# Performance work log

Measured on AMD Instinct MI355X. Metric: run time of the kernel, lower is better.

Reference implementation:

```python
import jax, jax.numpy as jnp
import numpy as np

N = 100000
E = 1000000
IN_C = 256
HID = 64
OUT = 64
NEG_SLOPE = 0.2


def setup_inputs() -> dict:
    key = jax.random.key(0)
    ks = jax.random.split(key, 12)
    x = jax.random.normal(ks[0], (N, IN_C), dtype=jnp.float32)
    edge_index = jax.random.randint(ks[1], (2, E), 0, N, dtype=jnp.int64)
    s = 1.0 / np.sqrt(IN_C)
    W1 = jax.random.uniform(ks[2], (IN_C, HID), jnp.float32, -s, s)
    a1_src = jax.random.uniform(ks[3], (HID,), jnp.float32, -s, s)
    a1_dst = jax.random.uniform(ks[4], (HID,), jnp.float32, -s, s)
    b1 = jnp.zeros((HID,), jnp.float32)
    s2 = 1.0 / np.sqrt(HID)
    W2 = jax.random.uniform(ks[5], (HID, OUT), jnp.float32, -s2, s2)
    a2_src = jax.random.uniform(ks[6], (OUT,), jnp.float32, -s2, s2)
    a2_dst = jax.random.uniform(ks[7], (OUT,), jnp.float32, -s2, s2)
    b2 = jnp.zeros((OUT,), jnp.float32)
    return {"x": x, "edge_index": edge_index, "W1": W1, "a1_src": a1_src,
            "a1_dst": a1_dst, "b1": b1, "W2": W2, "a2_src": a2_src,
            "a2_dst": a2_dst, "b2": b2}


def gat_conv(x, W, a_src, a_dst, b, src, dst):
    h = x @ W                              # [N, d]
    alpha_s = h @ a_src                    # [N]
    alpha_d = h @ a_dst                    # [N]
    e = jax.nn.leaky_relu(alpha_s[src] + alpha_d[dst], NEG_SLOPE)  # [E]
    # segment softmax over incoming edges of each destination node
    e_max = jax.lax.stop_gradient(jax.ops.segment_max(e, dst, num_segments=N))
    ex = jnp.exp(e - e_max[dst])
    denom = jax.ops.segment_sum(ex, dst, num_segments=N)
    alpha = ex / (denom[dst] + 1e-16)      # [E]
    out = jax.ops.segment_sum(alpha[:, None] * h[src], dst, num_segments=N)
    return out + b


def reference(x, edge_index, W1, a1_src, a1_dst, b1, W2, a2_src, a2_dst, b2):
    src, dst = edge_index[0], edge_index[1]
    # dropout(p=0.6) is identity in eval mode
    h = jax.nn.relu(gat_conv(x, W1, a1_src, a1_dst, b1, src, dst))
    out = gat_conv(h, W2, a2_src, a2_dst, b2, src, dst)
    return out
```

## Files before the change

kernel.cpp:

```cpp
#include <hip/hip_runtime.h>
#include <math.h>

#define HID 64
#define BSH 9
#define NPB 512
#define EPB 4096

typedef __attribute__((ext_vector_type(8))) short bf16x8;
typedef __attribute__((ext_vector_type(4))) float f32x4;
typedef __attribute__((ext_vector_type(4))) unsigned int u32x4;

__device__ __forceinline__ unsigned short f2bf(float f) {
    unsigned u = __float_as_uint(f);
    unsigned r = u + 0x7FFF + ((u >> 16) & 1);
    return (unsigned short)(r >> 16);
}
__device__ __forceinline__ float bf2f(unsigned short b) {
    return __uint_as_float(((unsigned)b) << 16);
}


__global__ __launch_bounds__(256) void bucket_count(const int* __restrict__ edst,
                                                    int* __restrict__ bcnt, int E_, int NB) {
    __shared__ int hist[256];
    int t = threadIdx.x;
    hist[t] = 0;
    __syncthreads();
    int base = blockIdx.x * EPB;
#pragma unroll
    for (int r = 0; r < EPB / 256; ++r) {
        int i = base + r * 256 + t;
        if (i < E_) atomicAdd(&hist[edst[i] >> BSH], 1);
    }
    __syncthreads();
    if (t < NB && hist[t]) atomicAdd(&bcnt[t], hist[t]);
}

__global__ __launch_bounds__(256) void scan_nb(const int* __restrict__ bcnt,
                                               int* __restrict__ bbase,
                                               int* __restrict__ bcur, int NB) {
    __shared__ int sd[256];
    int t = threadIdx.x;
    int v = (t < NB) ? bcnt[t] : 0;
    sd[t] = v;
    __syncthreads();
    for (int o = 1; o < 256; o <<= 1) {
        int u = (t >= o) ? sd[t - o] : 0;
        __syncthreads();
        sd[t] += u;
        __syncthreads();
    }
    int ex = sd[t] - v;
    if (t < NB) {
        bbase[t] = ex;
        bcur[t] = ex;
    }
    if (t == 0) bbase[NB] = sd[NB - 1];
}

__global__ __launch_bounds__(256) void bucket_scatter(const int* __restrict__ esrc,
                                                      const int* __restrict__ edst,
                                                      int* __restrict__ bcur,
                                                      int2* __restrict__ ebuf, int E_, int NB) {
    __shared__ int hist[256], chunk[256], lcur[256];
    int t = threadIdx.x;
    hist[t] = 0;
    lcur[t] = 0;
    __syncthreads();
    int base = blockIdx.x * EPB;
    int s[EPB / 256], d[EPB / 256];
#pragma unroll
    for (int r = 0; r < EPB / 256; ++r) {
        int i = base + r * 256 + t;
        if (i < E_) {
            s[r] = esrc[i];
            d[r] = edst[i];
            atomicAdd(&hist[d[r] >> BSH], 1);
        } else {
            d[r] = -1;
        }
    }
    __syncthreads();
    if (t < NB) chunk[t] = hist[t] ? atomicAdd(&bcur[t], hist[t]) : 0;
    __syncthreads();
#pragma unroll
    for (int r = 0; r < EPB / 256; ++r) {
        if (d[r] >= 0) {
            int b = d[r] >> BSH;
            int pos = chunk[b] + atomicAdd(&lcur[b], 1);
            ebuf[pos] = make_int2(s[r], d[r]);
        }
    }
}

__global__ __launch_bounds__(256) void csr_build(const int2* __restrict__ ebuf,
                                                 const int* __restrict__ bbase,
                                                 int* __restrict__ off,
                                                 int* __restrict__ srcs, int Nv, int NB) {
    __shared__ int dhist[NPB], dbase[NPB], psum[256];
    int b = blockIdx.x, t = threadIdx.x;
    int e0 = bbase[b], e1 = bbase[b + 1];
#pragma unroll
    for (int j = t; j < NPB; j += 256) dhist[j] = 0;
    __syncthreads();
    for (int i = e0 + t; i < e1; i += 256) {
        int d = ebuf[i].y;
        atomicAdd(&dhist[d & (NPB - 1)], 1);
    }
    __syncthreads();
    int a0 = dhist[2 * t], a1 = dhist[2 * t + 1];
    psum[t] = a0 + a1;
    __syncthreads();
    for (int o = 1; o < 256; o <<= 1) {
        int u = (t >= o) ? psum[t - o] : 0;
        __syncthreads();
        psum[t] += u;
        __syncthreads();
    }
    int ex = psum[t] - (a0 + a1);
    dbase[2 * t] = ex;
    dbase[2 * t + 1] = ex + a0;
    __syncthreads();
    for (int j = t; j < NPB; j += 256) {
        int node = (b << BSH) + j;
        if (node < Nv) off[node] = e0 + dbase[j];
    }
    if (b == NB - 1 && t == 0) off[Nv] = e1;
    __syncthreads();
    for (int i = e0 + t; i < e1; i += 256) {
        int2 p = ebuf[i];
        int pos = atomicAdd(&dbase[p.y & (NPB - 1)], 1);
        srcs[e0 + pos] = p.x;
    }
}


__global__ __launch_bounds__(256) void wt_kernel(const float* __restrict__ W,
                                                 unsigned short* __restrict__ Wt, int K) {
    int t = threadIdx.x;
    int k = blockIdx.x * 4 + (t >> 6);
    int n = t & 63;
    if (k < K) Wt[(size_t)n * K + k] = f2bf(W[(size_t)k * 64 + n]);
}


template <int K, bool BF16IN>
__global__ __launch_bounds__(256) void gemm_mfma(const void* __restrict__ Xv,
                                                 const unsigned short* __restrict__ Wt,
                                                 const float* __restrict__ a_s,
                                                 const float* __restrict__ a_d,
                                                 unsigned short* __restrict__ C,
                                                 float* __restrict__ as_,
                                                 float* __restrict__ ad_, int Nrows) {
    constexpr int KPAD = K + 8;
    constexpr int XPAD = 72;
    __shared__ __align__(16) unsigned short Ws[64 * KPAD];
    __shared__ __align__(16) unsigned short Xs[128 * XPAD];

    const float* Xf = (const float*)Xv;
    const unsigned short* Xb = (const unsigned short*)Xv;

    int t = threadIdx.x;
    int n0 = blockIdx.x * 128;
    int lane = t & 63;
    int w = t >> 6;
    int m = lane & 15;
    int q = lane >> 4;
    int base = n0 + w * 32;

    constexpr int KC8 = K / 8;
    for (int i = t; i < 64 * KC8; i += 256) {
        int n = i / KC8;
        int kc = i % KC8;
        u32x4 v = *(const u32x4*)(Wt + (size_t)n * K + kc * 8);
        *(u32x4*)(&Ws[n * KPAD + kc * 8]) = v;
    }

    f32x4 acc[2][4];
#pragma unroll
    for (int mi = 0; mi < 2; ++mi)
#pragma unroll
        for (int ct = 0; ct < 4; ++ct) acc[mi][ct] = (f32x4){0.f, 0.f, 0.f, 0.f};

    for (int k0 = 0; k0 < K; k0 += 64) {
        if (!BF16IN) {
#pragma unroll
            for (int i = 0; i < 8; ++i) {
                int idx = i * 256 + t;
                int row = idx >> 4;
                int kq = (idx & 15) * 4;
                int gn = n0 + row;
                if (gn >= Nrows) gn = Nrows - 1;
                float4 v = *(const float4*)(Xf + (size_t)gn * K + k0 + kq);
                ushort4 bb;
                bb.x = f2bf(v.x); bb.y = f2bf(v.y); bb.z = f2bf(v.z); bb.w = f2bf(v.w);
                *(ushort4*)(&Xs[row * XPAD + kq]) = bb;
            }
        } else {
#pragma unroll
            for (int i = 0; i < 4; ++i) {
                int idx = i * 256 + t;
                int row = idx >> 3;
                int kq = (idx & 7) * 8;
                int gn = n0 + row;
                if (gn >= Nrows) gn = Nrows - 1;
                u32x4 v = *(const u32x4*)(Xb + (size_t)gn * K + k0 + kq);
                *(u32x4*)(&Xs[row * XPAD + kq]) = v;
            }
        }
        __syncthreads();
#pragma unroll
        for (int ks = 0; ks < 64; ks += 32) {
            bf16x8 a0 = *(const bf16x8*)(&Xs[(w * 32 + m) * XPAD + ks + q * 8]);
            bf16x8 a1 = *(const bf16x8*)(&Xs[(w * 32 + 16 + m) * XPAD + ks + q * 8]);
#pragma unroll
            for (int ct = 0; ct < 4; ++ct) {
                bf16x8 bv = *(const bf16x8*)(&Ws[(ct * 16 + m) * KPAD + k0 + ks + q * 8]);
                acc[0][ct] = __builtin_amdgcn_mfma_f32_16x16x32_bf16(a0, bv, acc[0][ct], 0, 0, 0);
                acc[1][ct] = __builtin_amdgcn_mfma_f32_16x16x32_bf16(a1, bv, acc[1][ct], 0, 0, 0);
            }
        }
        __syncthreads();
    }

    float sa0 = a_s[m], sa1 = a_s[16 + m], sa2 = a_s[32 + m], sa3 = a_s[48 + m];
    float da0 = a_d[m], da1 = a_d[16 + m], da2 = a_d[32 + m], da3 = a_d[48 + m];

#pragma unroll
    for (int mi = 0; mi < 2; ++mi) {
#pragma unroll
        for (int r = 0; r < 4; ++r) {
            int row = base + mi * 16 + q * 4 + r;
            if (row < Nrows) {
                size_t ro = (size_t)row * 64 + m;
                C[ro]      = f2bf(acc[mi][0][r]);
                C[ro + 16] = f2bf(acc[mi][1][r]);
                C[ro + 32] = f2bf(acc[mi][2][r]);
                C[ro + 48] = f2bf(acc[mi][3][r]);
            }
        }
        float vs[4], vd[4];
#pragma unroll
        for (int r = 0; r < 4; ++r) {
            float s = acc[mi][0][r] * sa0 + acc[mi][1][r] * sa1 +
                      acc[mi][2][r] * sa2 + acc[mi][3][r] * sa3;
            float d = acc[mi][0][r] * da0 + acc[mi][1][r] * da1 +
                      acc[mi][2][r] * da2 + acc[mi][3][r] * da3;
#pragma unroll
            for (int o = 1; o < 16; o <<= 1) {
                s += __shfl_xor(s, o);
                d += __shfl_xor(d, o);
            }
            vs[r] = s;
            vd[r] = d;
        }
        if (m < 4) {
            int row = base + mi * 16 + q * 4 + m;
            float wvs = (m == 0) ? vs[0] : (m == 1) ? vs[1] : (m == 2) ? vs[2] : vs[3];
            float wvd = (m == 0) ? vd[0] : (m == 1) ? vd[1] : (m == 2) ? vd[2] : vd[3];
            if (row < Nrows) {
                as_[row] = wvs;
                ad_[row] = wvd;
            }
        }
    }
}


template <bool RELU_BF16OUT>
__global__ __launch_bounds__(256) void agg_kernel(const unsigned short* __restrict__ H,
                                                  const float* __restrict__ as_,
                                                  const float* __restrict__ ad_,
                                                  const float* __restrict__ bias,
                                                  const int* __restrict__ off,
                                                  const int* __restrict__ srcs,
                                                  void* __restrict__ outp, int Nrows) {
    int d = blockIdx.x * 4 + (threadIdx.x >> 6);
    int lane = threadIdx.x & 63;
    if (d >= Nrows) return;
    int begin = off[d], end = off[d + 1];
    float adv = ad_[d];
    float acc = 0.f, lsum = 0.f;

    for (int bbase = begin; bbase < end; bbase += 64) {
        int cnt = end - bbase;
        if (cnt > 64) cnt = 64;
        int s = 0;
        float p = 0.f;
        if (lane < cnt) {
            s = srcs[bbase + lane];
            float x = as_[s] + adv;
            x = (x > 0.f) ? x : 0.2f * x;
            p = __expf(x);
        }
        lsum += p;
        int nb = (cnt + 7) & ~7;
        for (int j = 0; j < nb; j += 8) {
            float hv[8], pv[8];
#pragma unroll
            for (int u = 0; u < 8; ++u) {
                int su = __builtin_amdgcn_readlane(s, j + u);
                pv[u] = __uint_as_float(
                    (unsigned)__builtin_amdgcn_readlane((int)__float_as_uint(p), j + u));
                hv[u] = bf2f(H[(size_t)su * HID + lane]);
            }
#pragma unroll
            for (int u = 0; u < 8; ++u) acc += pv[u] * hv[u];
        }
    }
#pragma unroll
    for (int o = 32; o; o >>= 1) lsum += __shfl_xor(lsum, o);
    float o = acc / (lsum + 1e-16f) + bias[lane];
    if (RELU_BF16OUT) {
        ((unsigned short*)outp)[(size_t)d * HID + lane] = f2bf(fmaxf(o, 0.f));
    } else {
        ((float*)outp)[(size_t)d * HID + lane] = o;
    }
}


extern "C" void kernel_launch(void* const* d_in, const int* in_sizes, int n_in,
                              void* d_out, int out_size, void* d_ws, size_t ws_size,
                              hipStream_t stream) {
    const float* x      = (const float*)d_in[0];
    const int*   edge   = (const int*)d_in[1];
    const float* W1     = (const float*)d_in[2];
    const float* a1_src = (const float*)d_in[3];
    const float* a1_dst = (const float*)d_in[4];
    const float* b1     = (const float*)d_in[5];
    const float* W2     = (const float*)d_in[6];
    const float* a2_src = (const float*)d_in[7];
    const float* a2_dst = (const float*)d_in[8];
    const float* b2     = (const float*)d_in[9];
    float* out = (float*)d_out;

    const int N = in_sizes[0] / 256;
    const int E = in_sizes[1] / 2;
    const int IN_C = 256;
    const int NB = (N + NPB - 1) >> BSH;

    char* w = (char*)d_ws;
    auto alloc = [&](size_t bytes) {
        char* p = w;
        w += (bytes + 255) & ~(size_t)255;
        return p;
    };
    int*            off   = (int*)alloc((size_t)(N + 1) * 4);
    int*            srcs  = (int*)alloc((size_t)E * 4);
    int2*           ebuf  = (int2*)alloc((size_t)E * 8);
    int*            bcnt  = (int*)alloc(256 * 4);
    int*            bbase = (int*)alloc(257 * 4);
    int*            bcur  = (int*)alloc(256 * 4);
    unsigned short* h1    = (unsigned short*)alloc((size_t)N * HID * 2);
    unsigned short* hB    = (unsigned short*)alloc((size_t)N * HID * 2);
    float*          as_   = (float*)alloc((size_t)N * 4);
    float*          ad_   = (float*)alloc((size_t)N * 4);
    unsigned short* Wt1   = (unsigned short*)alloc((size_t)IN_C * 64 * 2);
    unsigned short* Wt2   = (unsigned short*)alloc((size_t)64 * 64 * 2);

    const int* esrc = edge;
    const int* edst = edge + E;

    hipMemsetAsync(bcnt, 0, 256 * 4, stream);

    int gbk = (E + EPB - 1) / EPB;
    bucket_count<<<gbk, 256, 0, stream>>>(edst, bcnt, E, NB);
    scan_nb<<<1, 256, 0, stream>>>(bcnt, bbase, bcur, NB);
    bucket_scatter<<<gbk, 256, 0, stream>>>(esrc, edst, bcur, ebuf, E, NB);
    csr_build<<<NB, 256, 0, stream>>>(ebuf, bbase, off, srcs, N, NB);

    wt_kernel<<<IN_C / 4, 256, 0, stream>>>(W1, Wt1, IN_C);
    wt_kernel<<<64 / 4, 256, 0, stream>>>(W2, Wt2, 64);

    int gblocks = (N + 127) / 128;
    int ablocks = (N + 3) / 4;

    gemm_mfma<256, false><<<gblocks, 256, 0, stream>>>(x, Wt1, a1_src, a1_dst, h1, as_, ad_, N);
    agg_kernel<true><<<ablocks, 256, 0, stream>>>(h1, as_, ad_, b1, off, srcs, hB, N);

    gemm_mfma<64, true><<<gblocks, 256, 0, stream>>>(hB, Wt2, a2_src, a2_dst, h1, as_, ad_, N);
    agg_kernel<false><<<ablocks, 256, 0, stream>>>(h1, as_, ad_, b2, off, srcs, out, N);
}
```

Baseline: 332.9 us.

## Use fixed-capacity edge buckets to drop count and scan passes in CSR build

```diff
diff --git a/kernel.cpp b/kernel.cpp
--- a/kernel.cpp
+++ b/kernel.cpp
@@ -5,6 +5,7 @@
 #define BSH 9
 #define NPB 512
 #define EPB 4096
+#define CAP 8192
 
 typedef __attribute__((ext_vector_type(8))) short bf16x8;
 typedef __attribute__((ext_vector_type(4))) float f32x4;
@@ -20,48 +21,10 @@
 }
 
 
-__global__ __launch_bounds__(256) void bucket_count(const int* __restrict__ edst,
-                                                    int* __restrict__ bcnt, int E_, int NB) {
-    __shared__ int hist[256];
-    int t = threadIdx.x;
-    hist[t] = 0;
-    __syncthreads();
-    int base = blockIdx.x * EPB;
-#pragma unroll
-    for (int r = 0; r < EPB / 256; ++r) {
-        int i = base + r * 256 + t;
-        if (i < E_) atomicAdd(&hist[edst[i] >> BSH], 1);
-    }
-    __syncthreads();
-    if (t < NB && hist[t]) atomicAdd(&bcnt[t], hist[t]);
-}
-
-__global__ __launch_bounds__(256) void scan_nb(const int* __restrict__ bcnt,
-                                               int* __restrict__ bbase,
-                                               int* __restrict__ bcur, int NB) {
-    __shared__ int sd[256];
-    int t = threadIdx.x;
-    int v = (t < NB) ? bcnt[t] : 0;
-    sd[t] = v;
-    __syncthreads();
-    for (int o = 1; o < 256; o <<= 1) {
-        int u = (t >= o) ? sd[t - o] : 0;
-        __syncthreads();
-        sd[t] += u;
-        __syncthreads();
-    }
-    int ex = sd[t] - v;
-    if (t < NB) {
-        bbase[t] = ex;
-        bcur[t] = ex;
-    }
-    if (t == 0) bbase[NB] = sd[NB - 1];
-}
-
 __global__ __launch_bounds__(256) void bucket_scatter(const int* __restrict__ esrc,
                                                       const int* __restrict__ edst,
-                                                      int* __restrict__ bcur,
-                                                      int2* __restrict__ ebuf, int E_, int NB) {
+                                                      int* __restrict__ bcnt,
+                                                      int* __restrict__ ebuf, int E_, int NB) {
     __shared__ int hist[256], chunk[256], lcur[256];
     int t = threadIdx.x;
     hist[t] = 0;
@@ -81,31 +44,31 @@
         }
     }
     __syncthreads();
-    if (t < NB) chunk[t] = hist[t] ? atomicAdd(&bcur[t], hist[t]) : 0;
+    if (t < NB) chunk[t] = hist[t] ? atomicAdd(&bcnt[t], hist[t]) : 0;
     __syncthreads();
 #pragma unroll
     for (int r = 0; r < EPB / 256; ++r) {
         if (d[r] >= 0) {
             int b = d[r] >> BSH;
             int pos = chunk[b] + atomicAdd(&lcur[b], 1);
-            ebuf[pos] = make_int2(s[r], d[r]);
-        }
-    }
-}
-
-__global__ __launch_bounds__(256) void csr_build(const int2* __restrict__ ebuf,
-                                                 const int* __restrict__ bbase,
-                                                 int* __restrict__ off,
-                                                 int* __restrict__ srcs, int Nv, int NB) {
+            ebuf[b * CAP + pos] = (s[r] << BSH) | (d[r] & (NPB - 1));
+        }
+    }
+}
+
+__global__ __launch_bounds__(256) void csr_build(const int* __restrict__ ebuf,
+                                                 const int* __restrict__ bcnt,
+                                                 int2* __restrict__ offs,
+                                                 int* __restrict__ srcs, int Nv) {
     __shared__ int dhist[NPB], dbase[NPB], psum[256];
     int b = blockIdx.x, t = threadIdx.x;
-    int e0 = bbase[b], e1 = bbase[b + 1];
+    int cnt = bcnt[b];
+    int e0 = b * CAP;
 #pragma unroll
     for (int j = t; j < NPB; j += 256) dhist[j] = 0;
     __syncthreads();
-    for (int i = e0 + t; i < e1; i += 256) {
-        int d = ebuf[i].y;
-        atomicAdd(&dhist[d & (NPB - 1)], 1);
+    for (int i = t; i < cnt; i += 256) {
+        atomicAdd(&dhist[ebuf[e0 + i] & (NPB - 1)], 1);
     }
     __syncthreads();
     int a0 = dhist[2 * t], a1 = dhist[2 * t + 1];
@@ -121,26 +84,37 @@
     dbase[2 * t] = ex;
     dbase[2 * t + 1] = ex + a0;
     __syncthreads();
+#pragma unroll
     for (int j = t; j < NPB; j += 256) {
         int node = (b << BSH) + j;
-        if (node < Nv) off[node] = e0 + dbase[j];
-    }
-    if (b == NB - 1 && t == 0) off[Nv] = e1;
-    __syncthreads();
-    for (int i = e0 + t; i < e1; i += 256) {
-        int2 p = ebuf[i];
-        int pos = atomicAdd(&dbase[p.y & (NPB - 1)], 1);
-        srcs[e0 + pos] = p.x;
-    }
-}
-
-
-__global__ __launch_bounds__(256) void wt_kernel(const float* __restrict__ W,
-                                                 unsigned short* __restrict__ Wt, int K) {
+        if (node < Nv) {
+            int beg = e0 + dbase[j];
+            offs[node] = make_int2(beg, beg + dhist[j]);
+        }
+    }
+    __syncthreads();
+    for (int i = t; i < cnt; i += 256) {
+        int e = ebuf[e0 + i];
+        int pos = atomicAdd(&dbase[e & (NPB - 1)], 1);
+        srcs[e0 + pos] = e >> BSH;
+    }
+}
+
+
+__global__ __launch_bounds__(256) void wt_kernel(const float* __restrict__ W1,
+                                                 const float* __restrict__ W2,
+                                                 unsigned short* __restrict__ Wt1,
+                                                 unsigned short* __restrict__ Wt2) {
     int t = threadIdx.x;
-    int k = blockIdx.x * 4 + (t >> 6);
+    int blk = blockIdx.x;
     int n = t & 63;
-    if (k < K) Wt[(size_t)n * K + k] = f2bf(W[(size_t)k * 64 + n]);
+    if (blk < 64) {
+        int k = blk * 4 + (t >> 6);
+        Wt1[(size_t)n * 256 + k] = f2bf(W1[(size_t)k * 64 + n]);
+    } else {
+        int k = (blk - 64) * 4 + (t >> 6);
+        Wt2[(size_t)n * 64 + k] = f2bf(W2[(size_t)k * 64 + n]);
+    }
 }
 
 
@@ -272,13 +246,14 @@
                                                   const float* __restrict__ as_,
                                                   const float* __restrict__ ad_,
                                                   const float* __restrict__ bias,
-                                                  const int* __restrict__ off,
+                                                  const int2* __restrict__ offs,
                                                   const int* __restrict__ srcs,
                                                   void* __restrict__ outp, int Nrows) {
     int d = blockIdx.x * 4 + (threadIdx.x >> 6);
     int lane = threadIdx.x & 63;
     if (d >= Nrows) return;
-    int begin = off[d], end = off[d + 1];
+    int2 oe = offs[d];
+    int begin = oe.x, end = oe.y;
     float adv = ad_[d];
     float acc = 0.f, lsum = 0.f;
 
@@ -345,12 +320,10 @@
         w += (bytes + 255) & ~(size_t)255;
         return p;
     };
-    int*            off   = (int*)alloc((size_t)(N + 1) * 4);
-    int*            srcs  = (int*)alloc((size_t)E * 4);
-    int2*           ebuf  = (int2*)alloc((size_t)E * 8);
+    int2*           offs  = (int2*)alloc((size_t)N * 8);
+    int*            srcs  = (int*)alloc((size_t)NB * CAP * 4);
+    int*            ebuf  = (int*)alloc((size_t)NB * CAP * 4);
     int*            bcnt  = (int*)alloc(256 * 4);
-    int*            bbase = (int*)alloc(257 * 4);
-    int*            bcur  = (int*)alloc(256 * 4);
     unsigned short* h1    = (unsigned short*)alloc((size_t)N * HID * 2);
     unsigned short* hB    = (unsigned short*)alloc((size_t)N * HID * 2);
     float*          as_   = (float*)alloc((size_t)N * 4);
@@ -363,21 +336,18 @@
 
     hipMemsetAsync(bcnt, 0, 256 * 4, stream);
 
+    wt_kernel<<<IN_C / 4 + 64 / 4, 256, 0, stream>>>(W1, W2, Wt1, Wt2);
+
     int gbk = (E + EPB - 1) / EPB;
-    bucket_count<<<gbk, 256, 0, stream>>>(edst, bcnt, E, NB);
-    scan_nb<<<1, 256, 0, stream>>>(bcnt, bbase, bcur, NB);
-    bucket_scatter<<<gbk, 256, 0, stream>>>(esrc, edst, bcur, ebuf, E, NB);
-    csr_build<<<NB, 256, 0, stream>>>(ebuf, bbase, off, srcs, N, NB);
-
-    wt_kernel<<<IN_C / 4, 256, 0, stream>>>(W1, Wt1, IN_C);
-    wt_kernel<<<64 / 4, 256, 0, stream>>>(W2, Wt2, 64);
+    bucket_scatter<<<gbk, 256, 0, stream>>>(esrc, edst, bcnt, ebuf, E, NB);
+    csr_build<<<NB, 256, 0, stream>>>(ebuf, bcnt, offs, srcs, N);
 
     int gblocks = (N + 127) / 128;
     int ablocks = (N + 3) / 4;
 
     gemm_mfma<256, false><<<gblocks, 256, 0, stream>>>(x, Wt1, a1_src, a1_dst, h1, as_, ad_, N);
-    agg_kernel<true><<<ablocks, 256, 0, stream>>>(h1, as_, ad_, b1, off, srcs, hB, N);
+    agg_kernel<true><<<ablocks, 256, 0, stream>>>(h1, as_, ad_, b1, offs, srcs, hB, N);
 
     gemm_mfma<64, true><<<gblocks, 256, 0, stream>>>(hB, Wt2, a2_src, a2_dst, h1, as_, ad_, N);
-    agg_kernel<false><<<ablocks, 256, 0, stream>>>(h1, as_, ad_, b2, off, srcs, out, N);
-}
+    agg_kernel<false><<<ablocks, 256, 0, stream>>>(h1, as_, ad_, b2, offs, srcs, out, N);
+}
```

Result: faster. 316.2 us (-5.0%).
